# Performance work log

Hardware: AMD Instinct MI355X
Metric: run time of the kernel (lower is better)

## Reference

```python
import jax, jax.numpy as jnp
import numpy as np

C_IN = 256
C_OUT = 256
NUM_HEADS = 4
C_HEAD = C_OUT // NUM_HEADS  # 64
ALPHA = 0.2
NEG_FILL = -9e15


def setup_inputs() -> dict:
    key = jax.random.key(0)
    k1, k2, k3, k4, k5 = jax.random.split(key, 5)
    B, N = 1, 4096
    node_feats = jax.random.normal(k1, (B, N, C_IN), dtype=jnp.float32)
    adj_matrix = jax.random.randint(k2, (B, N, N), 0, 2, dtype=jnp.int32)
    # xavier_uniform with gain=1.414 on projection weight (fan_in=C_IN, fan_out=C_OUT)
    lim_w = 1.414 * np.sqrt(6.0 / (C_IN + C_OUT))
    W = jax.random.uniform(k3, (C_IN, C_OUT), dtype=jnp.float32, minval=-lim_w, maxval=lim_w)
    b = jnp.zeros((C_OUT,), dtype=jnp.float32)
    lim_a = 1.414 * np.sqrt(6.0 / (NUM_HEADS + 2 * C_HEAD))
    a = jax.random.uniform(k4, (NUM_HEADS, 2 * C_HEAD), dtype=jnp.float32, minval=-lim_a, maxval=lim_a)
    return {"node_feats": node_feats, "adj_matrix": adj_matrix, "W": W, "b": b, "a": a}


def reference(node_feats, adj_matrix, W, b, a):
    B, N, _ = node_feats.shape
    # linear projection -> (B, N, H, C_HEAD)
    feats = (node_feats @ W + b).reshape(B, N, NUM_HEADS, C_HEAD)
    # attention logit for edge (i -> j): a_src . h_i + a_dst . h_j, per head
    a_src, a_dst = a[:, :C_HEAD], a[:, C_HEAD:]
    src = jnp.einsum('bnhc,hc->bnh', feats, a_src)  # indexed by row i
    dst = jnp.einsum('bnhc,hc->bnh', feats, a_dst)  # indexed by col j
    logits = src[:, :, None, :] + dst[:, None, :, :]  # (B, N, N, H)
    logits = jnp.where(logits >= 0, logits, ALPHA * logits)  # LeakyReLU(0.2)
    attn = jnp.where(adj_matrix[..., None] == 1, logits, NEG_FILL)
    probs = jax.nn.softmax(attn, axis=2)  # softmax over source nodes j
    out = jnp.einsum('bijh,bjhc->bihc', probs, feats)
    return out.reshape(B, N, NUM_HEADS * C_HEAD)  # concat heads
```

## Files before the change

kernel.cpp:

```cpp
#include <hip/hip_runtime.h>

#define NN 4096
#define C 256
#define NH 4
#define CH 64
#define JSPLIT 8
#define JSLICE (NN / JSPLIT)
#define NJT (JSLICE / 32)

typedef float f32x4 __attribute__((ext_vector_type(4)));
typedef __bf16 b16x8 __attribute__((ext_vector_type(8)));
typedef unsigned short u16x8 __attribute__((ext_vector_type(8)));
typedef unsigned int u32x4 __attribute__((ext_vector_type(4)));

__device__ inline float fast_exp2(float x) {
#if __has_builtin(__builtin_amdgcn_exp2f)
  return __builtin_amdgcn_exp2f(x);
#else
  return exp2f(x);
#endif
}

__device__ inline unsigned pack2bf(float f0, float f1) {
  unsigned u0 = __float_as_uint(f0) + 0x8000u;
  unsigned u1 = __float_as_uint(f1) + 0x8000u;
  return __builtin_amdgcn_perm(u1, u0, 0x07060302u);
}

__global__ __launch_bounds__(256) void k_prep(
    const int* __restrict__ adj, const float* __restrict__ X,
    const float* __restrict__ W, unsigned char* __restrict__ packed,
    unsigned short* __restrict__ Xbf, unsigned short* __restrict__ WT) {
  const int b = blockIdx.x, t = threadIdx.x;
  if (b < 8192) {
    const int idx = b * 256 + t;
    const int4 a0 = *(const int4*)(adj + (size_t)idx * 8);
    const int4 a1 = *(const int4*)(adj + (size_t)idx * 8 + 4);
    unsigned m = 0;
    m |= (a0.x != 0) ? 1u : 0u;   m |= (a0.y != 0) ? 2u : 0u;
    m |= (a0.z != 0) ? 4u : 0u;   m |= (a0.w != 0) ? 8u : 0u;
    m |= (a1.x != 0) ? 16u : 0u;  m |= (a1.y != 0) ? 32u : 0u;
    m |= (a1.z != 0) ? 64u : 0u;  m |= (a1.w != 0) ? 128u : 0u;
    packed[idx] = (unsigned char)m;
  } else if (b < 9216) {
    const int idx = (b - 8192) * 256 + t;
    const float4 v = ((const float4*)X)[idx];
    uint2 st;
    st.x = pack2bf(v.x, v.y);
    st.y = pack2bf(v.z, v.w);
    ((uint2*)Xbf)[idx] = st;
  } else {
    const int c = b - 9216;
    const float w = W[(size_t)t * C + c];
    WT[(size_t)c * C + t] = (unsigned short)((__float_as_uint(w) + 0x8000u) >> 16);
  }
}

__global__ __launch_bounds__(256) void k_feats(
    const unsigned short* __restrict__ Xbf, const unsigned short* __restrict__ WT,
    const float* __restrict__ bias, const float* __restrict__ av,
    unsigned short* __restrict__ featsT, float* __restrict__ srcv,
    float* __restrict__ dstT) {
  const int i0 = blockIdx.x * 16;
  const int h = threadIdx.x >> 6;
  const int lane = threadIdx.x & 63;
  const int q = lane >> 4, n = lane & 15;
  const int c0 = h * CH;

  const f32x4 zero = {0.f, 0.f, 0.f, 0.f};
  f32x4 acc[4];
#pragma unroll
  for (int g = 0; g < 4; ++g) acc[g] = zero;

  const unsigned short* ap = Xbf + (size_t)(i0 + n) * C + q * 8;
#pragma unroll
  for (int kt = 0; kt < 8; ++kt) {
    const b16x8 aF = __builtin_bit_cast(b16x8, *(const u16x8*)(ap + kt * 32));
#pragma unroll
    for (int g = 0; g < 4; ++g) {
      const b16x8 bF = __builtin_bit_cast(b16x8,
          *(const u16x8*)(WT + (size_t)(c0 + g * 16 + n) * C + kt * 32 + q * 8));
      acc[g] = __builtin_amdgcn_mfma_f32_16x16x32_bf16(aF, bF, acc[g], 0, 0, 0);
    }
  }

  float fb[4][4], asv[4], adv[4];
#pragma unroll
  for (int g = 0; g < 4; ++g) {
    const float bs = bias[c0 + g * 16 + n];
    asv[g] = av[h * 128 + g * 16 + n];
    adv[g] = av[h * 128 + 64 + g * 16 + n];
#pragma unroll
    for (int r = 0; r < 4; ++r) fb[g][r] = acc[g][r] + bs;
  }
#pragma unroll
  for (int g = 0; g < 4; ++g) {
    uint2 st;
    st.x = pack2bf(fb[g][0], fb[g][1]);
    st.y = pack2bf(fb[g][2], fb[g][3]);
    *(uint2*)(featsT + (size_t)(c0 + g * 16 + n) * NN + i0 + q * 4) = st;
  }
#pragma unroll
  for (int r = 0; r < 4; ++r) {
    float p = 0.f, d = 0.f;
#pragma unroll
    for (int g = 0; g < 4; ++g) {
      p = fmaf(fb[g][r], asv[g], p);
      d = fmaf(fb[g][r], adv[g], d);
    }
#pragma unroll
    for (int m = 1; m < 16; m <<= 1) {
      p += __shfl_xor(p, m);
      d += __shfl_xor(d, m);
    }
    if (n == 0) {
      const int row = i0 + q * 4 + r;
      srcv[(size_t)row * NH + h] = p;
      dstT[(size_t)h * NN + row] = d;
    }
  }
}

__global__ __launch_bounds__(256, 4) void k_attn(
    const unsigned char* __restrict__ packed,
    const unsigned short* __restrict__ featsT,
    const float* __restrict__ srcv, const float* __restrict__ dstT,
    _Float16* __restrict__ pacc, float* __restrict__ lpart) {
  const int slice = blockIdx.x;
  const int i0 = blockIdx.y * 32;
  const int h = threadIdx.x >> 6;
  const int lane = threadIdx.x & 63;
  const int q = lane >> 4, n = lane & 15;
  const int jbase = slice * JSLICE;

  const float LOG2E = 1.4426950408889634f;
  const int r0 = i0 + n, r1 = i0 + 16 + n;
  const float s0 = srcv[(size_t)r0 * NH + h];
  const float s1 = srcv[(size_t)r1 * NH + h];
  const float xm0 = s0 + 16.0f, xm1 = s1 + 16.0f;
  const float m20 = fmaxf(xm0, 0.2f * xm0) * LOG2E;
  const float m21 = fmaxf(xm1, 0.2f * xm1) * LOG2E;

  const f32x4 zero = {0.f, 0.f, 0.f, 0.f};
  f32x4 acc0[4], acc1[4], lacc0 = zero, lacc1 = zero;
#pragma unroll
  for (int g = 0; g < 4; ++g) { acc0[g] = zero; acc1[g] = zero; }

  u16x8 ou;
#pragma unroll
  for (int jj = 0; jj < 8; ++jj) ou[jj] = 0x3F80;
  const b16x8 ones = __builtin_bit_cast(b16x8, ou);

  const unsigned char* mp0 = packed + (size_t)r0 * 512 + (jbase >> 3) + q;
  const unsigned char* mp1 = mp0 + 16 * 512;
  const float* dp = dstT + (size_t)h * NN + jbase + q * 8;

  unsigned Mb0 = mp0[0], Mb1 = mp1[0];
  float4 d0 = *(const float4*)dp, d1 = *(const float4*)(dp + 4);

  for (int jt = 0; jt < NJT; ++jt) {
    const int nx = (jt + 1 < NJT) ? jt + 1 : jt;
    const unsigned Mb0n = mp0[nx * 4], Mb1n = mp1[nx * 4];
    const float4 d0n = *(const float4*)(dp + nx * 32);
    const float4 d1n = *(const float4*)(dp + nx * 32 + 4);

    const int jq = jbase + jt * 32 + q * 8;
    b16x8 bF[4];
#pragma unroll
    for (int g = 0; g < 4; ++g)
      bF[g] = __builtin_bit_cast(b16x8,
          *(const u16x8*)(featsT + (size_t)(h * CH + g * 16 + n) * NN + jq));

    const float dv[8] = {d0.x, d0.y, d0.z, d0.w, d1.x, d1.y, d1.z, d1.w};
    u32x4 pk0, pk1;
#pragma unroll
    for (int p = 0; p < 4; ++p) {
      const int j0 = 2 * p, j1 = 2 * p + 1;
      float x, a;
      x = s0 + dv[j0]; a = fmaf(fmaxf(x, 0.2f * x), LOG2E, -m20);
      const float e00 = fast_exp2((Mb0 & (1u << j0)) ? a : -200.0f);
      x = s0 + dv[j1]; a = fmaf(fmaxf(x, 0.2f * x), LOG2E, -m20);
      const float e01 = fast_exp2((Mb0 & (1u << j1)) ? a : -200.0f);
      x = s1 + dv[j0]; a = fmaf(fmaxf(x, 0.2f * x), LOG2E, -m21);
      const float e10 = fast_exp2((Mb1 & (1u << j0)) ? a : -200.0f);
      x = s1 + dv[j1]; a = fmaf(fmaxf(x, 0.2f * x), LOG2E, -m21);
      const float e11 = fast_exp2((Mb1 & (1u << j1)) ? a : -200.0f);
      pk0[p] = pack2bf(e00, e01);
      pk1[p] = pack2bf(e10, e11);
    }
    const b16x8 E0 = __builtin_bit_cast(b16x8, pk0);
    const b16x8 E1 = __builtin_bit_cast(b16x8, pk1);
#pragma unroll
    for (int g = 0; g < 4; ++g) {
      acc0[g] = __builtin_amdgcn_mfma_f32_16x16x32_bf16(E0, bF[g], acc0[g], 0, 0, 0);
      acc1[g] = __builtin_amdgcn_mfma_f32_16x16x32_bf16(E1, bF[g], acc1[g], 0, 0, 0);
    }
    lacc0 = __builtin_amdgcn_mfma_f32_16x16x32_bf16(E0, ones, lacc0, 0, 0, 0);
    lacc1 = __builtin_amdgcn_mfma_f32_16x16x32_bf16(E1, ones, lacc1, 0, 0, 0);
    Mb0 = Mb0n; Mb1 = Mb1n; d0 = d0n; d1 = d1n;
  }

#pragma unroll
  for (int g = 0; g < 4; ++g)
#pragma unroll
    for (int r = 0; r < 4; ++r) {
      const int col = h * CH + g * 16 + n;
      pacc[((size_t)slice * NN + i0 + q * 4 + r) * C + col] = (_Float16)acc0[g][r];
      pacc[((size_t)slice * NN + i0 + 16 + q * 4 + r) * C + col] = (_Float16)acc1[g][r];
    }
  if (n == 0) {
#pragma unroll
    for (int r = 0; r < 4; ++r) {
      lpart[((size_t)slice * NN + i0 + q * 4 + r) * NH + h] = lacc0[r];
      lpart[((size_t)slice * NN + i0 + 16 + q * 4 + r) * NH + h] = lacc1[r];
    }
  }
}

__global__ __launch_bounds__(256) void k_final(
    const _Float16* __restrict__ pacc, const float* __restrict__ lpart,
    float* __restrict__ out) {
  const int i = blockIdx.x;
  const int c = threadIdx.x;
  const int h = c >> 6;
  float l = 0.f, sa = 0.f;
#pragma unroll
  for (int sp = 0; sp < JSPLIT; ++sp) {
    l += lpart[((size_t)sp * NN + i) * NH + h];
    sa += (float)pacc[((size_t)sp * NN + i) * C + c];
  }
  out[(size_t)i * C + c] = sa / l;
}

extern "C" void kernel_launch(void* const* d_in, const int* in_sizes, int n_in,
                              void* d_out, int out_size, void* d_ws, size_t ws_size,
                              hipStream_t stream) {
  const float* nf   = (const float*)d_in[0];
  const int* adj    = (const int*)d_in[1];
  const float* W    = (const float*)d_in[2];
  const float* bias = (const float*)d_in[3];
  const float* av   = (const float*)d_in[4];
  float* out = (float*)d_out;

  char* ws = (char*)d_ws;
  unsigned char* packed  = (unsigned char*)ws;
  unsigned short* Xbf    = (unsigned short*)(ws + (2u << 20));
  unsigned short* WT     = (unsigned short*)(ws + (4u << 20));
  unsigned short* featsT = (unsigned short*)(ws + (4u << 20) + (256u << 10));
  float* srcv  = (float*)(ws + (6u << 20) + (256u << 10));
  float* dstT  = (float*)(ws + (6u << 20) + (320u << 10));
  float* lpart = (float*)(ws + (6u << 20) + (384u << 10));
  _Float16* pacc = (_Float16*)(ws + (8u << 20));

  k_prep<<<9472, 256, 0, stream>>>(adj, nf, W, packed, Xbf, WT);
  k_feats<<<NN / 16, 256, 0, stream>>>(Xbf, WT, bias, av, featsT, srcv, dstT);
  dim3 g2(JSPLIT, NN / 32);
  k_attn<<<g2, 256, 0, stream>>>(packed, featsT, srcv, dstT, pacc, lpart);
  k_final<<<NN, 256, 0, stream>>>(pacc, lpart, out);
}
```

Measured before the change: 165.3 us.

## Pre-swizzle feats into MFMA fragment layout and fold LeakyReLU into precomputed dst terms

k_feats now writes projected features directly in the per-lane MFMA B-fragment order, so each k_attn lane reads one contiguous 16-byte chunk per tile instead of a strided row of featsT. It also stores dst pre-scaled by log2e together with its 0.2-scaled copy, which turns LeakyReLU plus the exponent setup into two adds and a max per element. Adjacency mask bytes are loaded once per block as 16-byte vectors and spread across lanes with shuffles, and the j loop is fully unrolled. This cuts memory transactions and ALU work in the attention loop, at the cost of doubling the dst buffer and adding shuffle instructions and register pressure from the unrolling.

```diff
diff --git a/kernel.cpp b/kernel.cpp
--- a/kernel.cpp
+++ b/kernel.cpp
@@ -59,13 +59,14 @@
 __global__ __launch_bounds__(256) void k_feats(
     const unsigned short* __restrict__ Xbf, const unsigned short* __restrict__ WT,
     const float* __restrict__ bias, const float* __restrict__ av,
-    unsigned short* __restrict__ featsT, float* __restrict__ srcv,
-    float* __restrict__ dstT) {
+    unsigned short* __restrict__ F, float* __restrict__ srcv,
+    float2* __restrict__ dstT2) {
   const int i0 = blockIdx.x * 16;
   const int h = threadIdx.x >> 6;
   const int lane = threadIdx.x & 63;
   const int q = lane >> 4, n = lane & 15;
   const int c0 = h * CH;
+  const float LOG2E = 1.4426950408889634f;
 
   const f32x4 zero = {0.f, 0.f, 0.f, 0.f};
   f32x4 acc[4];
@@ -93,12 +94,14 @@
 #pragma unroll
     for (int r = 0; r < 4; ++r) fb[g][r] = acc[g][r] + bs;
   }
+  const int jt = i0 >> 5, half = (i0 >> 4) & 1;
+  const int qp = half * 2 + (q >> 1);
 #pragma unroll
   for (int g = 0; g < 4; ++g) {
     uint2 st;
     st.x = pack2bf(fb[g][0], fb[g][1]);
     st.y = pack2bf(fb[g][2], fb[g][3]);
-    *(uint2*)(featsT + (size_t)(c0 + g * 16 + n) * NN + i0 + q * 4) = st;
+    *(uint2*)(F + ((size_t)((jt * NH + h) * 4 + g)) * 512 + (qp * 16 + n) * 8 + 4 * (q & 1)) = st;
   }
 #pragma unroll
   for (int r = 0; r < 4; ++r) {
@@ -116,15 +119,16 @@
     if (n == 0) {
       const int row = i0 + q * 4 + r;
       srcv[(size_t)row * NH + h] = p;
-      dstT[(size_t)h * NN + row] = d;
+      const float dL = d * LOG2E;
+      dstT2[(size_t)h * NN + row] = make_float2(dL, 0.2f * dL);
     }
   }
 }
 
 __global__ __launch_bounds__(256, 4) void k_attn(
     const unsigned char* __restrict__ packed,
-    const unsigned short* __restrict__ featsT,
-    const float* __restrict__ srcv, const float* __restrict__ dstT,
+    const unsigned short* __restrict__ F,
+    const float* __restrict__ srcv, const float2* __restrict__ dstT2,
     _Float16* __restrict__ pacc, float* __restrict__ lpart) {
   const int slice = blockIdx.x;
   const int i0 = blockIdx.y * 32;
@@ -140,6 +144,8 @@
   const float xm0 = s0 + 16.0f, xm1 = s1 + 16.0f;
   const float m20 = fmaxf(xm0, 0.2f * xm0) * LOG2E;
   const float m21 = fmaxf(xm1, 0.2f * xm1) * LOG2E;
+  const float u0 = fmaf(s0, LOG2E, -m20), w0 = fmaf(0.2f * s0, LOG2E, -m20);
+  const float u1 = fmaf(s1, LOG2E, -m21), w1 = fmaf(0.2f * s1, LOG2E, -m21);
 
   const f32x4 zero = {0.f, 0.f, 0.f, 0.f};
   f32x4 acc0[4], acc1[4], lacc0 = zero, lacc1 = zero;
@@ -151,53 +157,57 @@
   for (int jj = 0; jj < 8; ++jj) ou[jj] = 0x3F80;
   const b16x8 ones = __builtin_bit_cast(b16x8, ou);
 
-  const unsigned char* mp0 = packed + (size_t)r0 * 512 + (jbase >> 3) + q;
-  const unsigned char* mp1 = mp0 + 16 * 512;
-  const float* dp = dstT + (size_t)h * NN + jbase + q * 8;
-
-  unsigned Mb0 = mp0[0], Mb1 = mp1[0];
-  float4 d0 = *(const float4*)dp, d1 = *(const float4*)(dp + 4);
-
-  for (int jt = 0; jt < NJT; ++jt) {
-    const int nx = (jt + 1 < NJT) ? jt + 1 : jt;
-    const unsigned Mb0n = mp0[nx * 4], Mb1n = mp1[nx * 4];
-    const float4 d0n = *(const float4*)(dp + nx * 32);
-    const float4 d1n = *(const float4*)(dp + nx * 32 + 4);
-
-    const int jq = jbase + jt * 32 + q * 8;
-    b16x8 bF[4];
-#pragma unroll
-    for (int g = 0; g < 4; ++g)
-      bF[g] = __builtin_bit_cast(b16x8,
-          *(const u16x8*)(featsT + (size_t)(h * CH + g * 16 + n) * NN + jq));
-
-    const float dv[8] = {d0.x, d0.y, d0.z, d0.w, d1.x, d1.y, d1.z, d1.w};
-    u32x4 pk0, pk1;
-#pragma unroll
-    for (int p = 0; p < 4; ++p) {
-      const int j0 = 2 * p, j1 = 2 * p + 1;
-      float x, a;
-      x = s0 + dv[j0]; a = fmaf(fmaxf(x, 0.2f * x), LOG2E, -m20);
-      const float e00 = fast_exp2((Mb0 & (1u << j0)) ? a : -200.0f);
-      x = s0 + dv[j1]; a = fmaf(fmaxf(x, 0.2f * x), LOG2E, -m20);
-      const float e01 = fast_exp2((Mb0 & (1u << j1)) ? a : -200.0f);
-      x = s1 + dv[j0]; a = fmaf(fmaxf(x, 0.2f * x), LOG2E, -m21);
-      const float e10 = fast_exp2((Mb1 & (1u << j0)) ? a : -200.0f);
-      x = s1 + dv[j1]; a = fmaf(fmaxf(x, 0.2f * x), LOG2E, -m21);
-      const float e11 = fast_exp2((Mb1 & (1u << j1)) ? a : -200.0f);
-      pk0[p] = pack2bf(e00, e01);
-      pk1[p] = pack2bf(e10, e11);
-    }
-    const b16x8 E0 = __builtin_bit_cast(b16x8, pk0);
-    const b16x8 E1 = __builtin_bit_cast(b16x8, pk1);
-#pragma unroll
-    for (int g = 0; g < 4; ++g) {
-      acc0[g] = __builtin_amdgcn_mfma_f32_16x16x32_bf16(E0, bF[g], acc0[g], 0, 0, 0);
-      acc1[g] = __builtin_amdgcn_mfma_f32_16x16x32_bf16(E1, bF[g], acc1[g], 0, 0, 0);
-    }
-    lacc0 = __builtin_amdgcn_mfma_f32_16x16x32_bf16(E0, ones, lacc0, 0, 0, 0);
-    lacc1 = __builtin_amdgcn_mfma_f32_16x16x32_bf16(E1, ones, lacc1, 0, 0, 0);
-    Mb0 = Mb0n; Mb1 = Mb1n; d0 = d0n; d1 = d1n;
+  const u32x4 m40 = *(const u32x4*)(packed + (size_t)r0 * 512 + (jbase >> 3) + q * 16);
+  const u32x4 m41 = *(const u32x4*)(packed + (size_t)r1 * 512 + (jbase >> 3) + q * 16);
+
+  const float* dp2 = (const float*)(dstT2 + (size_t)h * NN + jbase);
+  const unsigned short* fp = F + ((size_t)((jbase >> 5) * NH + h) * 4) * 512 + lane * 8;
+
+#pragma unroll
+  for (int a = 0; a < 4; ++a) {
+#pragma unroll
+    for (int b = 0; b < 4; ++b) {
+      const int jt = a * 4 + b;
+      b16x8 bF[4];
+#pragma unroll
+      for (int g = 0; g < 4; ++g)
+        bF[g] = __builtin_bit_cast(b16x8,
+            *(const u16x8*)(fp + (size_t)(jt * NH * 4 + g) * 512));
+
+      const unsigned Mb0 = (unsigned(__shfl((int)m40[b], a * 16 + n)) >> (q * 8)) & 0xffu;
+      const unsigned Mb1 = (unsigned(__shfl((int)m41[b], a * 16 + n)) >> (q * 8)) & 0xffu;
+
+      const float* dq = dp2 + jt * 64 + q * 16;
+      const float4 dd0 = *(const float4*)(dq);
+      const float4 dd1 = *(const float4*)(dq + 4);
+      const float4 dd2 = *(const float4*)(dq + 8);
+      const float4 dd3 = *(const float4*)(dq + 12);
+      const float4 dd[4] = {dd0, dd1, dd2, dd3};
+
+      u32x4 pk0, pk1;
+#pragma unroll
+      for (int k = 0; k < 4; ++k) {
+        const float a00 = fmaxf(dd[k].x + u0, dd[k].y + w0);
+        const float a01 = fmaxf(dd[k].z + u0, dd[k].w + w0);
+        const float a10 = fmaxf(dd[k].x + u1, dd[k].y + w1);
+        const float a11 = fmaxf(dd[k].z + u1, dd[k].w + w1);
+        const float e00 = fast_exp2((Mb0 & (1u << (2 * k))) ? a00 : -200.0f);
+        const float e01 = fast_exp2((Mb0 & (2u << (2 * k))) ? a01 : -200.0f);
+        const float e10 = fast_exp2((Mb1 & (1u << (2 * k))) ? a10 : -200.0f);
+        const float e11 = fast_exp2((Mb1 & (2u << (2 * k))) ? a11 : -200.0f);
+        pk0[k] = pack2bf(e00, e01);
+        pk1[k] = pack2bf(e10, e11);
+      }
+      const b16x8 E0 = __builtin_bit_cast(b16x8, pk0);
+      const b16x8 E1 = __builtin_bit_cast(b16x8, pk1);
+#pragma unroll
+      for (int g = 0; g < 4; ++g) {
+        acc0[g] = __builtin_amdgcn_mfma_f32_16x16x32_bf16(E0, bF[g], acc0[g], 0, 0, 0);
+        acc1[g] = __builtin_amdgcn_mfma_f32_16x16x32_bf16(E1, bF[g], acc1[g], 0, 0, 0);
+      }
+      lacc0 = __builtin_amdgcn_mfma_f32_16x16x32_bf16(E0, ones, lacc0, 0, 0, 0);
+      lacc1 = __builtin_amdgcn_mfma_f32_16x16x32_bf16(E1, ones, lacc1, 0, 0, 0);
+    }
   }
 
 #pragma unroll
@@ -246,15 +256,15 @@
   unsigned char* packed  = (unsigned char*)ws;
   unsigned short* Xbf    = (unsigned short*)(ws + (2u << 20));
   unsigned short* WT     = (unsigned short*)(ws + (4u << 20));
-  unsigned short* featsT = (unsigned short*)(ws + (4u << 20) + (256u << 10));
-  float* srcv  = (float*)(ws + (6u << 20) + (256u << 10));
-  float* dstT  = (float*)(ws + (6u << 20) + (320u << 10));
-  float* lpart = (float*)(ws + (6u << 20) + (384u << 10));
+  unsigned short* F      = (unsigned short*)(ws + (4u << 20) + (256u << 10));
+  float* srcv   = (float*)(ws + (6u << 20) + (256u << 10));
+  float2* dstT2 = (float2*)(ws + (6u << 20) + (320u << 10));
+  float* lpart  = (float*)(ws + (6u << 20) + (448u << 10));
   _Float16* pacc = (_Float16*)(ws + (8u << 20));
 
   k_prep<<<9472, 256, 0, stream>>>(adj, nf, W, packed, Xbf, WT);
-  k_feats<<<NN / 16, 256, 0, stream>>>(Xbf, WT, bias, av, featsT, srcv, dstT);
+  k_feats<<<NN / 16, 256, 0, stream>>>(Xbf, WT, bias, av, F, srcv, dstT2);
   dim3 g2(JSPLIT, NN / 32);
-  k_attn<<<g2, 256, 0, stream>>>(packed, featsT, srcv, dstT, pacc, lpart);
+  k_attn<<<g2, 256, 0, stream>>>(packed, F, srcv, dstT2, pacc, lpart);
   k_final<<<NN, 256, 0, stream>>>(pacc, lpart, out);
 }
```

Result: faster. 139.9 us (-15.4%).
